# Performance work log

Measured on AMD Instinct MI355X. Metric: run time of the kernel, lower is better.

## Reference

```python
import jax, jax.numpy as jnp
import numpy as np

HID = 1024
HEADS = 16
DH = HID // HEADS
SCALE = DH ** -0.5
L, B = 2048, 2


def setup_inputs() -> dict:
    key = jax.random.key(0)
    ks = jax.random.split(key, 16)
    inp = {
        "query": jax.random.normal(ks[0], (L, B, HID), jnp.float32),
        "key": jax.random.normal(ks[1], (L, B, HID), jnp.float32),
        "value": jax.random.normal(ks[2], (L, B, HID), jnp.float32),
        "mask": jax.random.randint(ks[3], (B, L), 0, 2).astype(bool),
    }
    # xavier-uniform linear weights (torch Linear stores [out, in]; y = x @ W.T + b)
    lim = (6.0 / (HID + HID)) ** 0.5
    for i, name in enumerate(["wq", "wk", "wv", "wfc"]):
        inp[name] = jax.random.uniform(ks[4 + i], (HID, HID), jnp.float32, -lim, lim)
    inp["bq"] = jnp.zeros((HID,), jnp.float32)
    inp["bk"] = jnp.zeros((HID,), jnp.float32)
    inp["bv"] = jnp.zeros((HID,), jnp.float32)
    inp["bfc"] = jnp.zeros((HID,), jnp.float32)
    inp["tao"] = jnp.full((HEADS,), 10.0, jnp.float32)
    return inp


def reference(query, key, value, mask, wq, bq, wk, bk, wv, bv, wfc, bfc, tao):
    # inputs arrive [L, B, D]; module transposes to [B, L, D]
    q = jnp.swapaxes(query, 0, 1)
    k = jnp.swapaxes(key, 0, 1)
    v = jnp.swapaxes(value, 0, 1)
    bsz, length, _ = q.shape

    def heads(x, w, b):
        y = x @ w.T + b                      # [B, L, D]
        return y.reshape(bsz, length, HEADS, DH).transpose(0, 2, 1, 3)  # [B, H, L, d]

    Q = heads(q, wq, bq)
    K = heads(k, wk, bk)
    V = heads(v, wv, bv)

    qk = jnp.einsum("bhqd,bhkd->bhqk", Q, K) * SCALE  # [B, H, L, L]

    # gaussian positional bias: -|i-j|^2/2 * tao_h^-4
    idx = jnp.arange(length, dtype=jnp.float32)
    dist = -0.5 * (idx[:, None] - idx[None, :]) ** 2          # [L, L]
    qk = qk + dist[None, None, :, :] * (tao ** -4)[None, :, None, None]

    qk = jnp.where(mask[:, None, None, :], -jnp.inf, qk)
    attn = jax.nn.softmax(qk, axis=-1)  # dropout is identity in eval mode

    x = jnp.einsum("bhqk,bhkd->bhqd", attn, V)            # [B, H, L, d]
    x = x.transpose(0, 2, 1, 3).reshape(bsz, length, HID)  # [B, L, D]
    x = x @ wfc.T + bfc
    return jnp.swapaxes(x, 0, 1)  # [L, B, D]
```

## Files before the change

### kernel.cpp

```cpp
#include <hip/hip_runtime.h>

#define LQ   2048
#define BQ   2
#define HID  1024
#define NH   16
#define DH   64
#define SCALE 0.125f
#define L2E  1.44269504088896f
#define C1   0.18033688011f
#define EXPOFF 23.0831206542f

using short8  = __attribute__((ext_vector_type(8))) short;
using ushort8 = __attribute__((ext_vector_type(8))) unsigned short;
using f32x4   = __attribute__((ext_vector_type(4))) float;
typedef unsigned short u16;
typedef __attribute__((ext_vector_type(2))) __bf16 bf16x2;

__device__ inline u16 f2bf(float x) {
    unsigned int u = __float_as_uint(x);
    u = (u + 0x7fffu + ((u >> 16) & 1u)) >> 16;
    return (u16)u;
}

#if defined(__has_builtin)
#if __has_builtin(__builtin_amdgcn_cvt_pk_bf16_f32)
#define HAVE_PKBF 1
#endif
#if __has_builtin(__builtin_amdgcn_exp2f)
#define HAVE_EXP2 1
#endif
#endif

__device__ inline unsigned int pkbf(float a, float b) {
#ifdef HAVE_PKBF
    bf16x2 r = __builtin_amdgcn_cvt_pk_bf16_f32(a, b);
    return __builtin_bit_cast(unsigned int, r);
#else
    return (unsigned int)f2bf(a) | ((unsigned int)f2bf(b) << 16);
#endif
}

__device__ inline float fexp2(float x) {
#ifdef HAVE_EXP2
    return __builtin_amdgcn_exp2f(x);
#else
    return exp2f(x);
#endif
}

__device__ inline void gl_lds16(const void* g, void* l) {
    __builtin_amdgcn_global_load_lds(
        (const __attribute__((address_space(1))) void*)g,
        (__attribute__((address_space(3))) void*)l, 16, 0, 0);
}

struct CastArgs {
    const float* s[7];
    u16* d[7];
    int n[7];
    const unsigned char* mraw;
    int* mout;
    int mn;
};

__global__ __launch_bounds__(256) void castw(CastArgs a) {
    const int y = blockIdx.y;
    const int t = threadIdx.x;
    if (y == 7) {
        if (blockIdx.x != 0) return;
        __shared__ int cnt;
        if (t == 0) cnt = 0;
        __syncthreads();
        int local = 0;
        for (int i = t; i < a.mn; i += 256)
            if ((i & 3) && a.mraw[i]) local++;
        atomicAdd(&cnt, local);
        __syncthreads();
        bool isInt32 = (cnt == 0);
        const int* mi = (const int*)a.mraw;
        for (int i = t; i < a.mn; i += 256)
            a.mout[i] = isInt32 ? mi[i] : (int)a.mraw[i];
        return;
    }
    const float* s = a.s[y];
    u16* d = a.d[y];
    const int n4 = a.n[y] >> 2;
    for (int i = blockIdx.x * 256 + t; i < n4; i += gridDim.x * 256) {
        float4 v = *(const float4*)(s + (size_t)i * 4);
        uint2 p;
        p.x = pkbf(v.x, v.y);
        p.y = pkbf(v.z, v.w);
        *(uint2*)(d + (size_t)i * 4) = p;
    }
}

struct QkvArgs {
    const u16* A[3];
    const u16* W[3];
    const float* bias[3];
    u16* out[3];
};

__global__ __launch_bounds__(256) void gemm_qkv(QkvArgs ga) {
    __shared__ u16 As[128][64];
    __shared__ u16 Bs[128][64];

    const int z = blockIdx.z;
    const u16* A = ga.A[z];
    const u16* W = ga.W[z];
    const float* bias = ga.bias[z];
    u16* outp = ga.out[z];

    const int t = threadIdx.x;
    const int m0 = blockIdx.x * 128;
    const int n0 = blockIdx.y * 128;
    const int lane = t & 63;
    const int lane15 = lane & 15;
    const int quad = lane >> 4;
    const int w = t >> 6;
    const int wm = (w >> 1) * 64;
    const int wn = (w & 1) * 64;

    const int lrow = lane >> 3;
    const int ch = (lane & 7) ^ ((lane >> 3) & 7);
    const u16* aS = A + (size_t)(m0 + 32 * w + lrow) * HID + 8 * ch;
    const u16* bS = W + (size_t)(n0 + 32 * w + lrow) * HID + 8 * ch;

    const int s0 = (quad ^ (lane15 & 7)) * 8;
    const int s1 = ((4 + quad) ^ (lane15 & 7)) * 8;

    f32x4 acc[4][4];
#pragma unroll
    for (int i = 0; i < 4; i++)
#pragma unroll
        for (int j = 0; j < 4; j++) acc[i][j] = (f32x4){0,0,0,0};

    for (int k0 = 0; k0 < HID; k0 += 64) {
        __syncthreads();
#pragma unroll
        for (int i = 0; i < 4; i++) {
            gl_lds16(aS + (size_t)(8 * i) * HID + k0, &As[32 * w + 8 * i][0]);
            gl_lds16(bS + (size_t)(8 * i) * HID + k0, &Bs[32 * w + 8 * i][0]);
        }
        __syncthreads();

        short8 af0[4], af1[4], bf0[4], bf1[4];
#pragma unroll
        for (int i = 0; i < 4; i++) {
            const u16* ar = &As[wm + i * 16 + lane15][0];
            const u16* br = &Bs[wn + i * 16 + lane15][0];
            af0[i] = *(const short8*)(ar + s0);
            af1[i] = *(const short8*)(ar + s1);
            bf0[i] = *(const short8*)(br + s0);
            bf1[i] = *(const short8*)(br + s1);
        }
#pragma unroll
        for (int mi = 0; mi < 4; mi++)
#pragma unroll
            for (int ni = 0; ni < 4; ni++) {
                acc[mi][ni] = __builtin_amdgcn_mfma_f32_16x16x32_bf16(af0[mi], bf0[ni], acc[mi][ni], 0, 0, 0);
                acc[mi][ni] = __builtin_amdgcn_mfma_f32_16x16x32_bf16(af1[mi], bf1[ni], acc[mi][ni], 0, 0, 0);
            }
    }

#pragma unroll
    for (int mi = 0; mi < 4; mi++) {
#pragma unroll
        for (int ni = 0; ni < 4; ni++) {
            const int n = n0 + wn + ni * 16 + lane15;
            const float bv = bias[n];
            const int h = n >> 6, d = n & 63;
#pragma unroll
            for (int r = 0; r < 4; r++) {
                const int m = m0 + wm + mi * 16 + quad * 4 + r;
                const float c = acc[mi][ni][r] + bv;
                const int b = m & 1, l = m >> 1;
                if (z < 2) {
                    outp[(((size_t)(b * NH + h)) * LQ + l) * DH + d] = f2bf(c);
                } else {
                    outp[(((size_t)(b * NH + h)) * DH + d) * LQ + l] = f2bf(c);
                }
            }
        }
    }
}

__global__ __launch_bounds__(256) void gemm_fc(const u16* __restrict__ A,
                                               const u16* __restrict__ W,
                                               const float* __restrict__ bias,
                                               float* __restrict__ outp) {
    __shared__ u16 As[128][64];
    __shared__ u16 Bs[64][64];

    const int t = threadIdx.x;
    const int m0 = blockIdx.x * 128;
    const int n0 = blockIdx.y * 64;
    const int lane = t & 63;
    const int lane15 = lane & 15;
    const int quad = lane >> 4;
    const int w = t >> 6;
    const int wm = (w >> 1) * 64;
    const int wn = (w & 1) * 32;

    const int lrow = lane >> 3;
    const int ch = (lane & 7) ^ ((lane >> 3) & 7);
    const u16* aS = A + (size_t)(m0 + 32 * w + lrow) * HID + 8 * ch;
    const u16* bS = W + (size_t)(n0 + 16 * w + lrow) * HID + 8 * ch;

    const int s0 = (quad ^ (lane15 & 7)) * 8;
    const int s1 = ((4 + quad) ^ (lane15 & 7)) * 8;

    f32x4 acc[4][2];
#pragma unroll
    for (int i = 0; i < 4; i++)
#pragma unroll
        for (int j = 0; j < 2; j++) acc[i][j] = (f32x4){0,0,0,0};

    for (int k0 = 0; k0 < HID; k0 += 64) {
        __syncthreads();
#pragma unroll
        for (int i = 0; i < 4; i++)
            gl_lds16(aS + (size_t)(8 * i) * HID + k0, &As[32 * w + 8 * i][0]);
#pragma unroll
        for (int i = 0; i < 2; i++)
            gl_lds16(bS + (size_t)(8 * i) * HID + k0, &Bs[16 * w + 8 * i][0]);
        __syncthreads();

        short8 af0[4], af1[4], bf0[2], bf1[2];
#pragma unroll
        for (int i = 0; i < 4; i++) {
            const u16* ar = &As[wm + i * 16 + lane15][0];
            af0[i] = *(const short8*)(ar + s0);
            af1[i] = *(const short8*)(ar + s1);
        }
#pragma unroll
        for (int j = 0; j < 2; j++) {
            const u16* br = &Bs[wn + j * 16 + lane15][0];
            bf0[j] = *(const short8*)(br + s0);
            bf1[j] = *(const short8*)(br + s1);
        }
#pragma unroll
        for (int mi = 0; mi < 4; mi++)
#pragma unroll
            for (int ni = 0; ni < 2; ni++) {
                acc[mi][ni] = __builtin_amdgcn_mfma_f32_16x16x32_bf16(af0[mi], bf0[ni], acc[mi][ni], 0, 0, 0);
                acc[mi][ni] = __builtin_amdgcn_mfma_f32_16x16x32_bf16(af1[mi], bf1[ni], acc[mi][ni], 0, 0, 0);
            }
    }

#pragma unroll
    for (int mi = 0; mi < 4; mi++) {
#pragma unroll
        for (int ni = 0; ni < 2; ni++) {
            const int n = n0 + wn + ni * 16 + lane15;
            const float bv = bias[n];
#pragma unroll
            for (int r = 0; r < 4; r++) {
                const int m = m0 + wm + mi * 16 + quad * 4 + r;
                outp[(size_t)m * HID + n] = acc[mi][ni][r] + bv;
            }
        }
    }
}

#define PSTR 72

__global__ __launch_bounds__(512) void attn_kernel(const u16* __restrict__ Qg,
                                                   const u16* __restrict__ Kg,
                                                   const u16* __restrict__ Vtg,
                                                   const int* __restrict__ maskI,
                                                   const float* __restrict__ tao,
                                                   u16* __restrict__ Xa) {
    __shared__ u16 Ks[128][64];
    __shared__ u16 Vt[64][128];
    __shared__ u16 PT[128][PSTR];
    __shared__ float smask[128];

    const int bh = blockIdx.x;
    const int q0 = blockIdx.y * 128;
    const int b = bh >> 4;
    const int h = bh & 15;
    const int t = threadIdx.x;
    const int w = t >> 6;
    const int lane = t & 63;
    const int lane15 = lane & 15;
    const int quad = lane >> 4;

    const u16* Kbase = Kg + (size_t)bh * LQ * DH;
    const u16* Vtbase = Vtg + (size_t)bh * DH * LQ;
    const int* mrow = maskI + b * LQ;

    const float tv = tao[h];
    const float t2 = tv * tv;
    const float nb = -0.5f / (t2 * t2);
    const float nb2 = nb * L2E;
    const float skipd2 = -40.0f / nb2;

    const int qrow = q0 + w * 16 + lane15;
    short8 qB0, qB1;
    {
        const u16* qp_ = Qg + ((size_t)bh * LQ + qrow) * DH + quad * 8;
        qB0 = *(const short8*)(qp_);
        qB1 = *(const short8*)(qp_ + 32);
    }

    const int krow = 8 * w + (lane >> 3);
    const int kch = (lane & 7) ^ ((lane >> 3) & 7);
    const u16* kS = Kbase + (size_t)krow * DH + 8 * kch;
    const int vrow = 4 * w + (lane >> 4);
    const int vch = (lane & 8) | ((lane & 7) ^ (vrow & 7));
    const u16* vS = Vtbase + (size_t)vrow * LQ + 8 * vch;
    u16* kD0 = &Ks[8 * w][0];
    u16* kD1 = &Ks[64 + 8 * w][0];
    u16* vD0 = &Vt[4 * w][0];
    u16* vD1 = &Vt[32 + 4 * w][0];

    const int s0 = (quad ^ (lane15 & 7)) * 8;
    const int s1 = ((4 + quad) ^ (lane15 & 7)) * 8;

    f32x4 O[4];
#pragma unroll
    for (int mt = 0; mt < 4; mt++) O[mt] = (f32x4){0,0,0,0};
    float l_ = 0.0f;

    const float ebase0 = (float)(qrow - quad * 4);
    const int prow = w * 16 + lane15;

    for (int k0 = 0; k0 < LQ; k0 += 128) {
        {
            int dmin = 0;
            if (k0 > q0 + 127) dmin = k0 - (q0 + 127);
            else if (k0 + 127 < q0) dmin = q0 - (k0 + 127);
            const float df = (float)dmin;
            if (df * df > skipd2) continue;
        }
        __syncthreads();
        gl_lds16(kS + (size_t)k0 * DH, kD0);
        gl_lds16(kS + (size_t)(k0 + 64) * DH, kD1);
        gl_lds16(vS + k0, vD0);
        gl_lds16(vS + (size_t)32 * LQ + k0, vD1);
        if (t < 128) smask[t] = mrow[k0 + t] ? -3.0e38f : -EXPOFF;
        __syncthreads();

#pragma unroll
        for (int hh = 0; hh < 2; hh++) {
            const int kbase = 64 * hh;
            f32x4 S[4];
#pragma unroll
            for (int kt = 0; kt < 4; kt++) {
                const u16* kr = &Ks[kbase + kt * 16 + lane15][0];
                const short8 ka = *(const short8*)(kr + s0);
                const short8 kb = *(const short8*)(kr + s1);
                S[kt] = __builtin_amdgcn_mfma_f32_16x16x32_bf16(ka, qB0, (f32x4){0,0,0,0}, 0, 0, 0);
                S[kt] = __builtin_amdgcn_mfma_f32_16x16x32_bf16(kb, qB1, S[kt], 0, 0, 0);
            }

            const float ebase = ebase0 - (float)(k0 + kbase);
            float lacc = 0.0f;
#pragma unroll
            for (int kt = 0; kt < 4; kt++) {
                const float4 sm4 = *(const float4*)&smask[kbase + kt * 16 + quad * 4];
                float p[4];
#pragma unroll
                for (int r = 0; r < 4; r++) {
                    const float d = ebase - (float)(kt * 16 + r);
                    const float tb = fmaf(nb2 * d, d, ((const float*)&sm4)[r]);
                    p[r] = fexp2(fmaf(S[kt][r], C1, tb));
                    lacc += p[r];
                }
                uint2 pk2;
                pk2.x = pkbf(p[0], p[1]);
                pk2.y = pkbf(p[2], p[3]);
                *(uint2*)&PT[prow][kt * 16 + quad * 4] = pk2;
            }
            l_ += lacc;

            const short8 pB0 = *(const short8*)&PT[prow][quad * 8];
            const short8 pB1 = *(const short8*)&PT[prow][32 + quad * 8];
#pragma unroll
            for (int mt = 0; mt < 4; mt++) {
                const u16* vr = &Vt[mt * 16 + lane15][kbase];
                const short8 va = *(const short8*)(vr + s0);
                const short8 vb = *(const short8*)(vr + s1);
                O[mt] = __builtin_amdgcn_mfma_f32_16x16x32_bf16(va, pB0, O[mt], 0, 0, 0);
                O[mt] = __builtin_amdgcn_mfma_f32_16x16x32_bf16(vb, pB1, O[mt], 0, 0, 0);
            }
        }
    }

    l_ += __shfl_xor(l_, 16, 64);
    l_ += __shfl_xor(l_, 32, 64);

    {
        const float inv = 1.0f / l_;
        u16* dst = Xa + ((size_t)qrow * BQ + b) * HID + h * DH;
#pragma unroll
        for (int mt = 0; mt < 4; mt++) {
            uint2 pk2;
            pk2.x = pkbf(O[mt][0] * inv, O[mt][1] * inv);
            pk2.y = pkbf(O[mt][2] * inv, O[mt][3] * inv);
            *(uint2*)(dst + mt * 16 + quad * 4) = pk2;
        }
    }
}

extern "C" void kernel_launch(void* const* d_in, const int* in_sizes, int n_in,
                              void* d_out, int out_size, void* d_ws, size_t ws_size,
                              hipStream_t stream) {
    const float* q    = (const float*)d_in[0];
    const float* k    = (const float*)d_in[1];
    const float* v    = (const float*)d_in[2];
    const void*  mask = d_in[3];
    const float* wq   = (const float*)d_in[4];
    const float* wk   = (const float*)d_in[5];
    const float* wv   = (const float*)d_in[6];
    const float* wfc  = (const float*)d_in[7];
    const float* bq   = (const float*)d_in[8];
    const float* bk   = (const float*)d_in[9];
    const float* bv   = (const float*)d_in[10];
    const float* bfc  = (const float*)d_in[11];
    const float* tao  = (const float*)d_in[12];

    const size_t NE = (size_t)LQ * BQ * HID;
    const size_t NW = (size_t)HID * HID;
    u16* base = (u16*)d_ws;
    u16* Qp    = base;
    u16* Kp    = base + NE;
    u16* Vtp   = base + 2 * NE;
    u16* Xa    = base + 3 * NE;
    u16* qbf   = base + 4 * NE;
    u16* kbf   = base + 5 * NE;
    u16* vbf   = base + 6 * NE;
    u16* wqbf  = base + 7 * NE;
    u16* wkbf  = wqbf + NW;
    u16* wvbf  = wkbf + NW;
    u16* wfcbf = wvbf + NW;
    int* maskI = (int*)(wfcbf + NW);

    CastArgs ca;
    ca.s[0] = q;   ca.d[0] = qbf;   ca.n[0] = (int)NE;
    ca.s[1] = k;   ca.d[1] = kbf;   ca.n[1] = (int)NE;
    ca.s[2] = v;   ca.d[2] = vbf;   ca.n[2] = (int)NE;
    ca.s[3] = wq;  ca.d[3] = wqbf;  ca.n[3] = (int)NW;
    ca.s[4] = wk;  ca.d[4] = wkbf;  ca.n[4] = (int)NW;
    ca.s[5] = wv;  ca.d[5] = wvbf;  ca.n[5] = (int)NW;
    ca.s[6] = wfc; ca.d[6] = wfcbf; ca.n[6] = (int)NW;
    ca.mraw = (const unsigned char*)mask;
    ca.mout = maskI;
    ca.mn = BQ * LQ;
    castw<<<dim3(256, 8), 256, 0, stream>>>(ca);

    QkvArgs ga;
    ga.A[0] = qbf;  ga.W[0] = wqbf;  ga.bias[0] = bq;  ga.out[0] = Qp;
    ga.A[1] = kbf;  ga.W[1] = wkbf;  ga.bias[1] = bk;  ga.out[1] = Kp;
    ga.A[2] = vbf;  ga.W[2] = wvbf;  ga.bias[2] = bv;  ga.out[2] = Vtp;
    gemm_qkv<<<dim3(32, 8, 3), 256, 0, stream>>>(ga);

    attn_kernel<<<dim3(32, 16), 512, 0, stream>>>(Qp, Kp, Vtp, maskI, tao, Xa);

    gemm_fc<<<dim3(32, 16), 256, 0, stream>>>(Xa, wfcbf, bfc, (float*)d_out);
}
```

Before: 231.3 us.

## Double-buffer LDS tiles in QKV and output projection GEMMs

Both projection GEMMs now use two LDS buffers. The next K-slice is prefetched via direct global-to-LDS loads while MFMAs run on the current slice, and one barrier per iteration replaces two. The goal is to hide global load latency behind matrix math. LDS use per block doubles, which may lower occupancy. Correctness relies on the compiler waiting for the async LDS loads before the barrier.

Result: no change. 230.1 us (-0.5%).

```diff
diff --git a/kernel.cpp b/kernel.cpp
--- a/kernel.cpp
+++ b/kernel.cpp
@@ -102,8 +102,8 @@
 };
 
 __global__ __launch_bounds__(256) void gemm_qkv(QkvArgs ga) {
-    __shared__ u16 As[128][64];
-    __shared__ u16 Bs[128][64];
+    __shared__ u16 As[2][128][64];
+    __shared__ u16 Bs[2][128][64];
 
     const int z = blockIdx.z;
     const u16* A = ga.A[z];
@@ -135,25 +135,32 @@
 #pragma unroll
         for (int j = 0; j < 4; j++) acc[i][j] = (f32x4){0,0,0,0};
 
+#pragma unroll
+    for (int i = 0; i < 4; i++) {
+        gl_lds16(aS + (size_t)(8 * i) * HID, &As[0][32 * w + 8 * i][0]);
+        gl_lds16(bS + (size_t)(8 * i) * HID, &Bs[0][32 * w + 8 * i][0]);
+    }
+    __syncthreads();
+
+    int p = 0;
     for (int k0 = 0; k0 < HID; k0 += 64) {
-        __syncthreads();
+        short8 af0[4], af1[4], bf0[4], bf1[4];
 #pragma unroll
         for (int i = 0; i < 4; i++) {
-            gl_lds16(aS + (size_t)(8 * i) * HID + k0, &As[32 * w + 8 * i][0]);
-            gl_lds16(bS + (size_t)(8 * i) * HID + k0, &Bs[32 * w + 8 * i][0]);
-        }
-        __syncthreads();
-
-        short8 af0[4], af1[4], bf0[4], bf1[4];
-#pragma unroll
-        for (int i = 0; i < 4; i++) {
-            const u16* ar = &As[wm + i * 16 + lane15][0];
-            const u16* br = &Bs[wn + i * 16 + lane15][0];
+            const u16* ar = &As[p][wm + i * 16 + lane15][0];
+            const u16* br = &Bs[p][wn + i * 16 + lane15][0];
             af0[i] = *(const short8*)(ar + s0);
             af1[i] = *(const short8*)(ar + s1);
             bf0[i] = *(const short8*)(br + s0);
             bf1[i] = *(const short8*)(br + s1);
         }
+        if (k0 + 64 < HID) {
+#pragma unroll
+            for (int i = 0; i < 4; i++) {
+                gl_lds16(aS + (size_t)(8 * i) * HID + (k0 + 64), &As[p ^ 1][32 * w + 8 * i][0]);
+                gl_lds16(bS + (size_t)(8 * i) * HID + (k0 + 64), &Bs[p ^ 1][32 * w + 8 * i][0]);
+            }
+        }
 #pragma unroll
         for (int mi = 0; mi < 4; mi++)
 #pragma unroll
@@ -161,6 +168,8 @@
                 acc[mi][ni] = __builtin_amdgcn_mfma_f32_16x16x32_bf16(af0[mi], bf0[ni], acc[mi][ni], 0, 0, 0);
                 acc[mi][ni] = __builtin_amdgcn_mfma_f32_16x16x32_bf16(af1[mi], bf1[ni], acc[mi][ni], 0, 0, 0);
             }
+        __syncthreads();
+        p ^= 1;
     }
 
 #pragma unroll
@@ -189,8 +198,8 @@
                                                const u16* __restrict__ W,
                                                const float* __restrict__ bias,
                                                float* __restrict__ outp) {
-    __shared__ u16 As[128][64];
-    __shared__ u16 Bs[64][64];
+    __shared__ u16 As[2][128][64];
+    __shared__ u16 Bs[2][64][64];
 
     const int t = threadIdx.x;
     const int m0 = blockIdx.x * 128;
@@ -216,28 +225,36 @@
 #pragma unroll
         for (int j = 0; j < 2; j++) acc[i][j] = (f32x4){0,0,0,0};
 
+#pragma unroll
+    for (int i = 0; i < 4; i++)
+        gl_lds16(aS + (size_t)(8 * i) * HID, &As[0][32 * w + 8 * i][0]);
+#pragma unroll
+    for (int i = 0; i < 2; i++)
+        gl_lds16(bS + (size_t)(8 * i) * HID, &Bs[0][16 * w + 8 * i][0]);
+    __syncthreads();
+
+    int p = 0;
     for (int k0 = 0; k0 < HID; k0 += 64) {
-        __syncthreads();
-#pragma unroll
-        for (int i = 0; i < 4; i++)
-            gl_lds16(aS + (size_t)(8 * i) * HID + k0, &As[32 * w + 8 * i][0]);
-#pragma unroll
-        for (int i = 0; i < 2; i++)
-            gl_lds16(bS + (size_t)(8 * i) * HID + k0, &Bs[16 * w + 8 * i][0]);
-        __syncthreads();
-
         short8 af0[4], af1[4], bf0[2], bf1[2];
 #pragma unroll
         for (int i = 0; i < 4; i++) {
-            const u16* ar = &As[wm + i * 16 + lane15][0];
+            const u16* ar = &As[p][wm + i * 16 + lane15][0];
             af0[i] = *(const short8*)(ar + s0);
             af1[i] = *(const short8*)(ar + s1);
         }
 #pragma unroll
         for (int j = 0; j < 2; j++) {
-            const u16* br = &Bs[wn + j * 16 + lane15][0];
+            const u16* br = &Bs[p][wn + j * 16 + lane15][0];
             bf0[j] = *(const short8*)(br + s0);
             bf1[j] = *(const short8*)(br + s1);
+        }
+        if (k0 + 64 < HID) {
+#pragma unroll
+            for (int i = 0; i < 4; i++)
+                gl_lds16(aS + (size_t)(8 * i) * HID + (k0 + 64), &As[p ^ 1][32 * w + 8 * i][0]);
+#pragma unroll
+            for (int i = 0; i < 2; i++)
+                gl_lds16(bS + (size_t)(8 * i) * HID + (k0 + 64), &Bs[p ^ 1][16 * w + 8 * i][0]);
         }
 #pragma unroll
         for (int mi = 0; mi < 4; mi++)
@@ -246,6 +263,8 @@
                 acc[mi][ni] = __builtin_amdgcn_mfma_f32_16x16x32_bf16(af0[mi], bf0[ni], acc[mi][ni], 0, 0, 0);
                 acc[mi][ni] = __builtin_amdgcn_mfma_f32_16x16x32_bf16(af1[mi], bf1[ni], acc[mi][ni], 0, 0, 0);
             }
+        __syncthreads();
+        p ^= 1;
     }
 
 #pragma unroll
```
